# Kernel tuning notes

Hardware: AMD Instinct MI355X
Metric: run time of the kernel (lower is better)

Reference implementation:

```python
import jax, jax.numpy as jnp
import numpy as np
from jax import lax

B_SZ, SEQ, D_MODEL, D_STATE, DT_RANK = 4, 4096, 256, 16, 16


def setup_inputs() -> dict:
    key = jax.random.key(0)
    ks = jax.random.split(key, 12)
    d, n, r = D_MODEL, D_STATE, DT_RANK
    inp = {}
    inp["hidden_states"] = jax.random.normal(ks[0], (B_SZ, SEQ, d), jnp.float32)
    inp["in_proj_w"] = jax.random.normal(ks[1], (3 * d, d), jnp.float32) * (d ** -0.5)
    inp["x_proj_w"] = jax.random.normal(ks[2], (r + 2 * n, d), jnp.float32) * (d ** -0.5)
    s = r ** -0.5
    inp["dt_proj_w"] = jax.random.uniform(ks[3], (d, r), jnp.float32, -s, s)
    dt = jnp.exp(jax.random.uniform(ks[4], (d,), jnp.float32) * (np.log(0.1) - np.log(1e-3)) + np.log(1e-3))
    inp["dt_proj_b"] = dt + jnp.log(-jnp.expm1(-dt))  # inverse-softplus init
    inp["A_log"] = jnp.log(jnp.broadcast_to(jnp.arange(1, n + 1, dtype=jnp.float32), (d, n)))
    inp["D"] = jnp.ones((d,), jnp.float32)
    inp["out_proj1_w"] = jax.random.normal(ks[5], (d, d), jnp.float32) * (d ** -0.5)
    inp["conv_x_w"] = jax.random.normal(ks[6], (d, 1, 1), jnp.float32)
    inp["conv_x_b"] = jax.random.normal(ks[7], (d,), jnp.float32) * 0.1
    inp["conv_y_w"] = jax.random.normal(ks[8], (d, 1, 3), jnp.float32) * (3 ** -0.5)
    inp["conv_y_b"] = jax.random.normal(ks[9], (d,), jnp.float32) * 0.1
    inp["conv_z_w"] = jax.random.normal(ks[10], (d, 1, 5), jnp.float32) * (5 ** -0.5)
    inp["conv_z_b"] = jax.random.normal(ks[11], (d,), jnp.float32) * 0.1
    return inp


def _silu(x):
    return x * jax.nn.sigmoid(x)


def _dwconv(x, w, b):
    # x: (b, d, l); w: (d, 1, k) depthwise; 'same' padding (odd k)
    k = w.shape[-1]
    pad = (k - 1) // 2
    out = lax.conv_general_dilated(
        x, w, window_strides=(1,), padding=[(pad, pad)],
        dimension_numbers=("NCH", "OIH", "NCH"), feature_group_count=x.shape[1])
    return out + b[None, :, None]


def _selective_scan(u, delta, A, B, C, D, delta_bias):
    # u, delta: (b,d,l); A: (d,n); B,C: (b,n,l); D, delta_bias: (d,)
    delta = jax.nn.softplus(delta + delta_bias[None, :, None])
    dA = jnp.exp(jnp.einsum("bdl,dn->lbdn", delta, A))          # (l,b,d,n)
    dBu = jnp.einsum("bdl,bnl,bdl->lbdn", delta, B, u)           # (l,b,d,n)
    Ct = jnp.transpose(C, (2, 0, 1))                             # (l,b,n)

    def step(h, inp):
        dA_t, dBu_t, C_t = inp
        h = dA_t * h + dBu_t                                     # (b,d,n)
        y = jnp.einsum("bdn,bn->bd", h, C_t)
        return h, y

    h0 = jnp.zeros(u.shape[:2] + (A.shape[1],), u.dtype)
    _, ys = lax.scan(step, h0, (dA, dBu, Ct))                    # ys: (l,b,d)
    y = jnp.transpose(ys, (1, 2, 0))                             # (b,d,l)
    return y + D[None, :, None] * u


def reference(hidden_states, in_proj_w, x_proj_w, dt_proj_w, dt_proj_b, A_log, D,
              out_proj1_w, conv_x_w, conv_x_b, conv_y_w, conv_y_b, conv_z_w, conv_z_b):
    b, l, d = hidden_states.shape
    xyz = jnp.einsum("ble,de->bdl", hidden_states, in_proj_w)    # (b, 3d, l)
    x, y, z = jnp.split(xyz, 3, axis=1)                          # each (b,d,l)
    A = -jnp.exp(A_log.astype(jnp.float32))
    x = _silu(_dwconv(x, conv_x_w, conv_x_b))
    y = _silu(_dwconv(y, conv_y_w, conv_y_b))
    z = _silu(_dwconv(z, conv_z_w, conv_z_b))
    x_dbl = jnp.einsum("bdl,ed->ble", x, x_proj_w)               # (b,l,r+2n)
    dt_r, Bm, Cm = jnp.split(x_dbl, [DT_RANK, DT_RANK + D_STATE], axis=-1)
    # dt_proj applies bias here; selective_scan adds delta_bias again (faithful to source)
    dt = jnp.einsum("blr,dr->bdl", dt_r, dt_proj_w) + dt_proj_b[None, :, None]
    Bm = jnp.transpose(Bm, (0, 2, 1))                            # (b,n,l)
    Cm = jnp.transpose(Cm, (0, 2, 1))
    p = _selective_scan(x, dt, A, Bm, Cm, D.astype(jnp.float32), dt_proj_b.astype(jnp.float32))
    p = jnp.transpose(p, (0, 2, 1))                              # (b,l,d)
    y = jnp.transpose(y, (0, 2, 1))
    z = jnp.transpose(z, (0, 2, 1))
    l1 = jnp.einsum("bld,ed->ble", p * y, out_proj1_w)
    l2 = l1 * z
    l2 = _dwconv(jnp.transpose(l2, (0, 2, 1)), conv_x_w, conv_x_b)
    return jnp.transpose(l2, (0, 2, 1))                          # (b,l,d)
```

## Files before the change

### kernel.cpp

```cpp
#include <hip/hip_runtime.h>
#include <hip/hip_bf16.h>
#include <math.h>

typedef __hip_bfloat16 bf16;
typedef __attribute__((ext_vector_type(8))) short bf16x8;
typedef __attribute__((ext_vector_type(4))) float f32x4;

#define B_SZ 4
#define SEQ  4096
#define DM   256
#define NST  16
#define NCHK 64
#define LC   (SEQ/NCHK)
#define MT   (B_SZ*SEQ)
#define CT   4

__device__ __forceinline__ float silu_f(float v){ return v / (1.f + __expf(-v)); }
__device__ __forceinline__ float softplus_f(float v){
  return (v > 15.f) ? v : __logf(1.f + __expf(v));
}
__device__ __forceinline__ short f2bf(float f){
  union { bf16 h; short s; } u; u.h = __float2bfloat16(f); return u.s;
}
__device__ __forceinline__ float bf2f(short s){
  union { unsigned int i; float f; } v;
  v.i = ((unsigned int)(unsigned short)s) << 16; return v.f;
}
__device__ __forceinline__ float4 bf4_to_f4(uint2 q){
  float4 f;
  f.x = bf2f((short)(q.x & 0xffffu)); f.y = bf2f((short)(q.x >> 16));
  f.z = bf2f((short)(q.y & 0xffffu)); f.w = bf2f((short)(q.y >> 16));
  return f;
}
__device__ __forceinline__ short4 f4_to_bf4(float4 f){
  short4 s; s.x = f2bf(f.x); s.y = f2bf(f.y); s.z = f2bf(f.z); s.w = f2bf(f.w);
  return s;
}

template<int CTRL>
__device__ __forceinline__ float dpp_add_step(float v){
  int x = __builtin_amdgcn_update_dpp(0, __float_as_int(v), CTRL, 0xf, 0xf, true);
  return v + __int_as_float(x);
}

template<int EPI, bool A2M, bool ABF, bool OBF>
__global__ __launch_bounds__(256)
void mfma_gemm_k(const void* __restrict__ Av, const void* __restrict__ A2v,
                 const float* __restrict__ Bw, void* __restrict__ Outv,
                 int N, int K,
                 const float* __restrict__ bias, const short* __restrict__ zc,
                 const float* __restrict__ cwx)
{
  constexpr int BM = 128, BN = 128, BK = 32, LDP = 40;
  __shared__ short As[BM * LDP];
  __shared__ short Bs[BN * LDP];
  const int tid  = threadIdx.x;
  const int wave = tid >> 6, lane = tid & 63;
  const int quad = lane >> 4, l16 = lane & 15;
  const int wm = (wave & 1) * 64, wn = (wave >> 1) * 64;
  const int m0 = blockIdx.x * BM, n0 = blockIdx.y * BN;
  const int srow = tid >> 3;
  const int skq  = (tid & 7) * 4;

  f32x4 acc[4][4] = {};

  for (int k0 = 0; k0 < K; k0 += BK) {
    #pragma unroll
    for (int p = 0; p < 4; p++) {
      int row = p * 32 + srow;
      size_t ga = (size_t)(m0 + row) * K + k0 + skq;
      float4 q;
      if constexpr (ABF) q = bf4_to_f4(*(const uint2*)((const short*)Av + ga));
      else               q = *(const float4*)((const float*)Av + ga);
      if constexpr (A2M) {
        float4 r = bf4_to_f4(*(const uint2*)((const short*)A2v + ga));
        q.x *= r.x; q.y *= r.y; q.z *= r.z; q.w *= r.w;
      }
      *(short4*)&As[row * LDP + skq] = f4_to_bf4(q);
      size_t gb = (size_t)(n0 + row) * K + k0 + skq;
      *(short4*)&Bs[row * LDP + skq] = f4_to_bf4(*(const float4*)(Bw + gb));
    }
    __syncthreads();
    bf16x8 fa[4], fb[4];
    #pragma unroll
    for (int i = 0; i < 4; i++) {
      fa[i] = *(const bf16x8*)&As[(wm + i * 16 + l16) * LDP + quad * 8];
      fb[i] = *(const bf16x8*)&Bs[(wn + i * 16 + l16) * LDP + quad * 8];
    }
    #pragma unroll
    for (int i = 0; i < 4; i++)
      #pragma unroll
      for (int j = 0; j < 4; j++)
        acc[i][j] = __builtin_amdgcn_mfma_f32_16x16x32_bf16(fa[i], fb[j], acc[i][j], 0, 0, 0);
    __syncthreads();
  }

  #pragma unroll
  for (int i = 0; i < 4; i++) {
    #pragma unroll
    for (int j = 0; j < 4; j++) {
      int n = n0 + wn + j * 16 + l16;
      #pragma unroll
      for (int r = 0; r < 4; r++) {
        int m = m0 + wm + i * 16 + quad * 4 + r;
        float v = acc[i][j][r];
        if constexpr (EPI == 2)
          v = v * bf2f(zc[(size_t)m * N + n]) * cwx[n] + bias[n];
        if constexpr (OBF) ((short*)Outv)[(size_t)m * N + n] = f2bf(v);
        else               ((float*)Outv)[(size_t)m * N + n] = v;
      }
    }
  }
}

__global__ __launch_bounds__(256)
void gemm34_k(const short* __restrict__ xcb,
              const float* __restrict__ Bw,
              const float* __restrict__ wdt,
              const float* __restrict__ bdt,
              float* __restrict__ xdbl,
              float* __restrict__ dtv)
{
  constexpr int TM = 64, TK = 16, NN = 48;
  __shared__ __align__(16) float As[TK][TM + 4];
  __shared__ __align__(16) float Bs[TK][TM + 4];
  __shared__ __align__(16) float dt_s[TM][20];
  __shared__ __align__(16) float wdt_s[256][20];
  const int tid = threadIdx.x;
  const int tn = tid & 15, tm = tid >> 4;
  const int m0 = blockIdx.x * TM;
  float acc[4][4] = {};
  const int ml = tid >> 2;
  const int kq = (tid & 3) << 2;

  {
    float4 q0 = *(const float4*)&wdt[tid * 16 + 0];
    float4 q1 = *(const float4*)&wdt[tid * 16 + 4];
    float4 q2 = *(const float4*)&wdt[tid * 16 + 8];
    float4 q3 = *(const float4*)&wdt[tid * 16 + 12];
    *(float4*)&wdt_s[tid][0]  = q0;
    *(float4*)&wdt_s[tid][4]  = q1;
    *(float4*)&wdt_s[tid][8]  = q2;
    *(float4*)&wdt_s[tid][12] = q3;
  }

  for (int k0 = 0; k0 < 256; k0 += TK) {
    {
      size_t off = (size_t)(m0 + ml) * 256 + k0 + kq;
      float4 q = bf4_to_f4(*(const uint2*)(xcb + off));
      As[kq+0][ml] = q.x; As[kq+1][ml] = q.y; As[kq+2][ml] = q.z; As[kq+3][ml] = q.w;
    }
    {
      float v0 = 0.f, v1 = 0.f, v2 = 0.f, v3 = 0.f;
      if (ml < NN) {
        float4 q = *(const float4*)(Bw + (size_t)ml * 256 + k0 + kq);
        v0 = q.x; v1 = q.y; v2 = q.z; v3 = q.w;
      }
      Bs[kq+0][ml] = v0; Bs[kq+1][ml] = v1; Bs[kq+2][ml] = v2; Bs[kq+3][ml] = v3;
    }
    __syncthreads();
    #pragma unroll
    for (int k = 0; k < TK; k++) {
      float4 av = *(const float4*)&As[k][tm << 2];
      float4 bv = *(const float4*)&Bs[k][tn << 2];
      float a[4] = {av.x, av.y, av.z, av.w};
      float b[4] = {bv.x, bv.y, bv.z, bv.w};
      #pragma unroll
      for (int i = 0; i < 4; i++)
        #pragma unroll
        for (int j = 0; j < 4; j++)
          acc[i][j] = fmaf(a[i], b[j], acc[i][j]);
    }
    __syncthreads();
  }

  #pragma unroll
  for (int i = 0; i < 4; i++) {
    int m = m0 + (tm << 2) + i;
    #pragma unroll
    for (int j = 0; j < 4; j++) {
      int n = (tn << 2) + j;
      float v = acc[i][j];
      if (n < NN) xdbl[(size_t)m * NN + n] = v;
      if (tn < 4) dt_s[(tm << 2) + i][n] = v;
    }
  }
  __syncthreads();

  const int c0 = tid & 63, rg = tid >> 6;
  float w[4][16];
  float bb[4];
  #pragma unroll
  for (int cc = 0; cc < 4; cc++) {
    int col = cc * 64 + c0;
    #pragma unroll
    for (int q = 0; q < 4; q++) {
      float4 t = *(const float4*)&wdt_s[col][q * 4];
      w[cc][q*4+0] = t.x; w[cc][q*4+1] = t.y; w[cc][q*4+2] = t.z; w[cc][q*4+3] = t.w;
    }
    bb[cc] = 2.f * bdt[col];
  }
  #pragma unroll
  for (int rr = 0; rr < 16; rr++) {
    int row = rg * 16 + rr;
    float dr[16];
    #pragma unroll
    for (int q = 0; q < 4; q++) {
      float4 t = *(const float4*)&dt_s[row][q * 4];
      dr[q*4+0] = t.x; dr[q*4+1] = t.y; dr[q*4+2] = t.z; dr[q*4+3] = t.w;
    }
    #pragma unroll
    for (int cc = 0; cc < 4; cc++) {
      float s = bb[cc];
      #pragma unroll
      for (int k = 0; k < 16; k++) s = fmaf(dr[k], w[cc][k], s);
      dtv[(size_t)(m0 + row) * 256 + cc * 64 + c0] = softplus_f(s);
    }
  }
}

__global__ __launch_bounds__(256)
void conv_silu_k(const short* __restrict__ xyzb,
                 const float* __restrict__ wx, const float* __restrict__ bx,
                 const float* __restrict__ wy, const float* __restrict__ by,
                 const float* __restrict__ wz, const float* __restrict__ bz,
                 short* __restrict__ xcb, short* __restrict__ ycb,
                 short* __restrict__ zcb)
{
  int idx = blockIdx.x * 256 + threadIdx.x;
  int c4 = idx % 192;
  int lt = idx / 192;
  int row0 = lt * CT;
  int l0 = row0 & (SEQ - 1);

  float4 win[CT + 4];
  #pragma unroll
  for (int i = 0; i < CT + 4; i++) {
    int l = l0 + i - 2;
    if (l >= 0 && l < SEQ)
      win[i] = bf4_to_f4(*(const uint2*)(xyzb + (size_t)(row0 + i - 2) * 768 + c4 * 4));
    else
      win[i] = make_float4(0.f, 0.f, 0.f, 0.f);
  }

  if (c4 < 64) {
    int d = c4 * 4;
    float4 w  = *(const float4*)&wx[d];
    float4 bb = *(const float4*)&bx[d];
    #pragma unroll
    for (int t = 0; t < CT; t++) {
      float4 v = win[t + 2], o;
      o.x = silu_f(fmaf(v.x, w.x, bb.x));
      o.y = silu_f(fmaf(v.y, w.y, bb.y));
      o.z = silu_f(fmaf(v.z, w.z, bb.z));
      o.w = silu_f(fmaf(v.w, w.w, bb.w));
      *(short4*)&xcb[(size_t)(row0 + t) * 256 + d] = f4_to_bf4(o);
    }
  } else if (c4 < 128) {
    int d = (c4 - 64) * 4;
    float wq[4][3];
    #pragma unroll
    for (int q = 0; q < 4; q++)
      #pragma unroll
      for (int j = 0; j < 3; j++) wq[q][j] = wy[(d + q) * 3 + j];
    float4 bb = *(const float4*)&by[d];
    #pragma unroll
    for (int t = 0; t < CT; t++) {
      float a0 = bb.x, a1 = bb.y, a2 = bb.z, a3 = bb.w;
      #pragma unroll
      for (int j = 0; j < 3; j++) {
        float4 v = win[t + 1 + j];
        a0 = fmaf(v.x, wq[0][j], a0);
        a1 = fmaf(v.y, wq[1][j], a1);
        a2 = fmaf(v.z, wq[2][j], a2);
        a3 = fmaf(v.w, wq[3][j], a3);
      }
      float4 o; o.x = silu_f(a0); o.y = silu_f(a1); o.z = silu_f(a2); o.w = silu_f(a3);
      *(short4*)&ycb[(size_t)(row0 + t) * 256 + d] = f4_to_bf4(o);
    }
  } else {
    int d = (c4 - 128) * 4;
    float wq[4][5];
    #pragma unroll
    for (int q = 0; q < 4; q++)
      #pragma unroll
      for (int j = 0; j < 5; j++) wq[q][j] = wz[(d + q) * 5 + j];
    float4 bb = *(const float4*)&bz[d];
    #pragma unroll
    for (int t = 0; t < CT; t++) {
      float a0 = bb.x, a1 = bb.y, a2 = bb.z, a3 = bb.w;
      #pragma unroll
      for (int j = 0; j < 5; j++) {
        float4 v = win[t + j];
        a0 = fmaf(v.x, wq[0][j], a0);
        a1 = fmaf(v.y, wq[1][j], a1);
        a2 = fmaf(v.z, wq[2][j], a2);
        a3 = fmaf(v.w, wq[3][j], a3);
      }
      float4 o; o.x = silu_f(a0); o.y = silu_f(a1); o.z = silu_f(a2); o.w = silu_f(a3);
      *(short4*)&zcb[(size_t)(row0 + t) * 256 + d] = f4_to_bf4(o);
    }
  }
}

template<bool PASSC>
__global__ __launch_bounds__(256)
void scan_k(const short* __restrict__ xcb,
            const float* __restrict__ dtv,
            const float* __restrict__ xdbl,
            const float* __restrict__ A_log,
            const float* __restrict__ Dp,
            const float* __restrict__ Hstart,
            float* __restrict__ Pbuf, float* __restrict__ hfbuf,
            short* __restrict__ poutb)
{
  __shared__ __align__(16) float2 du2_s[16 * 66];
  __shared__ __align__(16) float2 BC_s [PASSC ? 16 * 66 : 2];
  __shared__ __align__(16) float  Bc_s [PASSC ? 4 : 16 * 68];
  __shared__ __align__(16) float  y_s  [PASSC ? 16 * 68 : 4];
  const int tid = threadIdx.x;
  const int n = tid & 15, dl = tid >> 4;
  const int ch = blockIdx.x;
  const int d0 = blockIdx.y * 16;
  const int b  = blockIdx.z;
  const int d  = d0 + dl;
  const int t0 = ch * LC;
  const size_t brow = (size_t)b * SEQ;

  float u_r[4];
  #pragma unroll
  for (int i = 0; i < 4; i++) {
    int t = (tid >> 4) + i * 16;
    int dd = tid & 15;
    size_t row = brow + t0 + t;
    float uval = bf2f(xcb[row * 256 + d0 + dd]);
    float dval = dtv[row * 256 + d0 + dd];
    du2_s[dd * 66 + t] = make_float2(dval, dval * uval);
    if constexpr (PASSC) {
      BC_s[dd * 66 + t] = make_float2(xdbl[row * 48 + 16 + dd],
                                      xdbl[row * 48 + 32 + dd]);
      u_r[i] = uval;
    } else {
      Bc_s[dd * 68 + t] = xdbl[row * 48 + 16 + dd];
    }
  }
  __syncthreads();

  const float A_dn = -__expf(A_log[d * NST + n]);
  const size_t cidx = (((size_t)b * DM + d) * NST + n) * NCHK + ch;

  float h = PASSC ? Hstart[cidx] : 0.f;
  float P = 1.f;
  for (int t4 = 0; t4 < LC; t4 += 4) {
    float4 a = *(const float4*)&du2_s[dl * 66 + t4];
    float4 c = *(const float4*)&du2_s[dl * 66 + t4 + 2];
    float dA[4], du[4];
    dA[0] = __expf(a.x * A_dn); du[0] = a.y;
    dA[1] = __expf(a.z * A_dn); du[1] = a.w;
    dA[2] = __expf(c.x * A_dn); du[2] = c.y;
    dA[3] = __expf(c.z * A_dn); du[3] = c.w;
    if constexpr (!PASSC) {
      float4 f = *(const float4*)&Bc_s[n * 68 + t4];
      float Bv[4] = {f.x, f.y, f.z, f.w};
      #pragma unroll
      for (int j = 0; j < 4; j++) {
        h = fmaf(dA[j], h, du[j] * Bv[j]);
        P *= dA[j];
      }
    } else {
      float4 e = *(const float4*)&BC_s[n * 66 + t4];
      float4 g = *(const float4*)&BC_s[n * 66 + t4 + 2];
      float Bv[4] = {e.x, e.z, g.x, g.z};
      float Cv[4] = {e.y, e.w, g.y, g.w};
      float yv[4];
      #pragma unroll
      for (int j = 0; j < 4; j++) {
        h = fmaf(dA[j], h, du[j] * Bv[j]);
        yv[j] = h * Cv[j];
      }
      #pragma unroll
      for (int j = 0; j < 4; j++) yv[j] = dpp_add_step<0x118>(yv[j]);
      #pragma unroll
      for (int j = 0; j < 4; j++) yv[j] = dpp_add_step<0x114>(yv[j]);
      #pragma unroll
      for (int j = 0; j < 4; j++) yv[j] = dpp_add_step<0x112>(yv[j]);
      #pragma unroll
      for (int j = 0; j < 4; j++) yv[j] = dpp_add_step<0x111>(yv[j]);
      if (n == 15)
        *(float4*)&y_s[dl * 68 + t4] = make_float4(yv[0], yv[1], yv[2], yv[3]);
    }
  }

  if constexpr (!PASSC) {
    Pbuf[cidx] = P;
    hfbuf[cidx] = h;
  } else {
    __syncthreads();
    const float Dval = Dp[d0 + n];
    #pragma unroll
    for (int i = 0; i < 4; i++) {
      int t = (tid >> 4) + i * 16;
      poutb[(brow + t0 + t) * 256 + d0 + n] =
          f2bf(fmaf(Dval, u_r[i], y_s[n * 68 + t]));
    }
  }
}

__global__ __launch_bounds__(256)
void scan_mid_k(const float* __restrict__ Pbuf, const float* __restrict__ hfbuf,
                float* __restrict__ Hstart)
{
  int tid = blockIdx.x * 256 + threadIdx.x;
  size_t base = (size_t)tid * NCHK;
  float H = 0.f;
  for (int c = 0; c < NCHK; c++) {
    Hstart[base + c] = H;
    H = Pbuf[base + c] * H + hfbuf[base + c];
  }
}

extern "C" void kernel_launch(void* const* d_in, const int* in_sizes, int n_in,
                              void* d_out, int out_size, void* d_ws, size_t ws_size,
                              hipStream_t stream)
{
  const float* hs    = (const float*)d_in[0];
  const float* w_in  = (const float*)d_in[1];
  const float* w_xp  = (const float*)d_in[2];
  const float* w_dt  = (const float*)d_in[3];
  const float* b_dt  = (const float*)d_in[4];
  const float* A_log = (const float*)d_in[5];
  const float* Dp    = (const float*)d_in[6];
  const float* w_o1  = (const float*)d_in[7];
  const float* cwx   = (const float*)d_in[8];
  const float* cbx   = (const float*)d_in[9];
  const float* cwy   = (const float*)d_in[10];
  const float* cby   = (const float*)d_in[11];
  const float* cwz   = (const float*)d_in[12];
  const float* cbz   = (const float*)d_in[13];

  char* wsb = (char*)d_ws;
  short* xyzb = (short*)wsb;
  short* xcb  = (short*)(wsb + (size_t)MT * 768 * 2);
  short* ycb  = xcb + (size_t)MT * 256;
  short* zcb  = ycb + (size_t)MT * 256;
  short* pbufb= zcb + (size_t)MT * 256;
  float* xdbl = (float*)(pbufb + (size_t)MT * 256);
  float* dtv  = xdbl + (size_t)MT * 48;
  float* Pb   = dtv  + (size_t)MT * 256;
  float* hf   = Pb   + (size_t)B_SZ * DM * NST * NCHK;
  float* Hs   = hf   + (size_t)B_SZ * DM * NST * NCHK;

  dim3 blk(256);

  mfma_gemm_k<0, false, false, true><<<dim3(MT / 128, 768 / 128), blk, 0, stream>>>(
      hs, nullptr, w_in, xyzb, 768, 256, nullptr, nullptr, nullptr);

  conv_silu_k<<<dim3((MT / CT) * 192 / 256), blk, 0, stream>>>(
      xyzb, cwx, cbx, cwy, cby, cwz, cbz, xcb, ycb, zcb);

  gemm34_k<<<dim3(MT / 64), blk, 0, stream>>>(
      xcb, w_xp, w_dt, b_dt, xdbl, dtv);

  scan_k<false><<<dim3(NCHK, DM / 16, B_SZ), blk, 0, stream>>>(
      xcb, dtv, xdbl, A_log, Dp, nullptr, Pb, hf, nullptr);
  scan_mid_k<<<dim3((B_SZ * DM * NST) / 256), blk, 0, stream>>>(Pb, hf, Hs);
  scan_k<true><<<dim3(NCHK, DM / 16, B_SZ), blk, 0, stream>>>(
      xcb, dtv, xdbl, A_log, Dp, Hs, nullptr, nullptr, pbufb);

  mfma_gemm_k<2, true, true, false><<<dim3(MT / 128, 256 / 128), blk, 0, stream>>>(
      pbufb, ycb, w_o1, (float*)d_out, 256, 256, cbx, zcb, cwx);
}
```

Baseline: 219.3 us.

## Pre-convert GEMM weights to bf16, fuse y-gate into scan, shrink gemm34 tiles

A new small kernel converts the in-proj and out-proj weights to bf16 once per call. The MFMA GEMM then loads both operands with 16-byte copies and no per-tile conversion. The y gating multiply moves into the scan's output stage, so the final GEMM reads only one bf16 activation instead of two. gemm34 now uses 32-row tiles, doubling the grid for better occupancy, at the cost of reloading the weights more often and one extra kernel launch.

Result: faster. 208.6 us (-4.9%).

```diff
diff --git a/kernel.cpp b/kernel.cpp
--- a/kernel.cpp
+++ b/kernel.cpp
@@ -43,11 +43,25 @@
   return v + __int_as_float(x);
 }
 
-template<int EPI, bool A2M, bool ABF, bool OBF>
 __global__ __launch_bounds__(256)
-void mfma_gemm_k(const void* __restrict__ Av, const void* __restrict__ A2v,
-                 const float* __restrict__ Bw, void* __restrict__ Outv,
-                 int N, int K,
+void cvt_w_k(const float* __restrict__ w_in, const float* __restrict__ w_o1,
+             short* __restrict__ w_in_b, short* __restrict__ w_o1_b)
+{
+  int i = blockIdx.x * 256 + threadIdx.x;
+  if (i < 49152) {
+    float4 q = *(const float4*)&w_in[i * 4];
+    *(short4*)&w_in_b[i * 4] = f4_to_bf4(q);
+  } else {
+    int j = i - 49152;
+    float4 q = *(const float4*)&w_o1[j * 4];
+    *(short4*)&w_o1_b[j * 4] = f4_to_bf4(q);
+  }
+}
+
+template<int EPI, bool ABF, bool OBF>
+__global__ __launch_bounds__(256)
+void mfma_gemm_k(const void* __restrict__ Av, const short* __restrict__ Bw,
+                 void* __restrict__ Outv, int N, int K,
                  const float* __restrict__ bias, const short* __restrict__ zc,
                  const float* __restrict__ cwx)
 {
@@ -61,24 +75,35 @@
   const int m0 = blockIdx.x * BM, n0 = blockIdx.y * BN;
   const int srow = tid >> 3;
   const int skq  = (tid & 7) * 4;
+  const int crow = tid >> 2;
+  const int cck  = (tid & 3) * 8;
 
   f32x4 acc[4][4] = {};
 
   for (int k0 = 0; k0 < K; k0 += BK) {
-    #pragma unroll
-    for (int p = 0; p < 4; p++) {
-      int row = p * 32 + srow;
-      size_t ga = (size_t)(m0 + row) * K + k0 + skq;
-      float4 q;
-      if constexpr (ABF) q = bf4_to_f4(*(const uint2*)((const short*)Av + ga));
-      else               q = *(const float4*)((const float*)Av + ga);
-      if constexpr (A2M) {
-        float4 r = bf4_to_f4(*(const uint2*)((const short*)A2v + ga));
-        q.x *= r.x; q.y *= r.y; q.z *= r.z; q.w *= r.w;
-      }
-      *(short4*)&As[row * LDP + skq] = f4_to_bf4(q);
-      size_t gb = (size_t)(n0 + row) * K + k0 + skq;
-      *(short4*)&Bs[row * LDP + skq] = f4_to_bf4(*(const float4*)(Bw + gb));
+    if constexpr (ABF) {
+      #pragma unroll
+      for (int p = 0; p < 2; p++) {
+        int row = p * 64 + crow;
+        uint4 v = *(const uint4*)((const short*)Av + (size_t)(m0 + row) * K + k0 + cck);
+        *(uint4*)&As[row * LDP + cck] = v;
+      }
+    } else {
+      #pragma unroll
+      for (int p = 0; p < 4; p++) {
+        int row = p * 32 + srow;
+        size_t ga = (size_t)(m0 + row) * K + k0 + skq;
+        float4 q = *(const float4*)((const float*)Av + ga);
+        *(short4*)&As[row * LDP + skq] = f4_to_bf4(q);
+      }
+    }
+    {
+      #pragma unroll
+      for (int p = 0; p < 2; p++) {
+        int row = p * 64 + crow;
+        uint4 v = *(const uint4*)(Bw + (size_t)(n0 + row) * K + k0 + cck);
+        *(uint4*)&Bs[row * LDP + cck] = v;
+      }
     }
     __syncthreads();
     bf16x8 fa[4], fb[4];
@@ -121,17 +146,17 @@
               float* __restrict__ xdbl,
               float* __restrict__ dtv)
 {
-  constexpr int TM = 64, TK = 16, NN = 48;
+  constexpr int TM = 32, TK = 16, NN = 48;
   __shared__ __align__(16) float As[TK][TM + 4];
-  __shared__ __align__(16) float Bs[TK][TM + 4];
+  __shared__ __align__(16) float Bs[TK][64 + 4];
   __shared__ __align__(16) float dt_s[TM][20];
   __shared__ __align__(16) float wdt_s[256][20];
   const int tid = threadIdx.x;
   const int tn = tid & 15, tm = tid >> 4;
   const int m0 = blockIdx.x * TM;
-  float acc[4][4] = {};
-  const int ml = tid >> 2;
-  const int kq = (tid & 3) << 2;
+  float acc[2][4] = {};
+  const int mlA = tid >> 3, kdA = (tid & 7) * 2;
+  const int mlB = tid >> 2, kqB = (tid & 3) * 4;
 
   {
     float4 q0 = *(const float4*)&wdt[tid * 16 + 0];
@@ -146,27 +171,28 @@
 
   for (int k0 = 0; k0 < 256; k0 += TK) {
     {
-      size_t off = (size_t)(m0 + ml) * 256 + k0 + kq;
-      float4 q = bf4_to_f4(*(const uint2*)(xcb + off));
-      As[kq+0][ml] = q.x; As[kq+1][ml] = q.y; As[kq+2][ml] = q.z; As[kq+3][ml] = q.w;
+      size_t off = (size_t)(m0 + mlA) * 256 + k0 + kdA;
+      unsigned int v = *(const unsigned int*)(xcb + off);
+      As[kdA + 0][mlA] = bf2f((short)(v & 0xffffu));
+      As[kdA + 1][mlA] = bf2f((short)(v >> 16));
     }
     {
       float v0 = 0.f, v1 = 0.f, v2 = 0.f, v3 = 0.f;
-      if (ml < NN) {
-        float4 q = *(const float4*)(Bw + (size_t)ml * 256 + k0 + kq);
+      if (mlB < NN) {
+        float4 q = *(const float4*)(Bw + (size_t)mlB * 256 + k0 + kqB);
         v0 = q.x; v1 = q.y; v2 = q.z; v3 = q.w;
       }
-      Bs[kq+0][ml] = v0; Bs[kq+1][ml] = v1; Bs[kq+2][ml] = v2; Bs[kq+3][ml] = v3;
+      Bs[kqB+0][mlB] = v0; Bs[kqB+1][mlB] = v1; Bs[kqB+2][mlB] = v2; Bs[kqB+3][mlB] = v3;
     }
     __syncthreads();
     #pragma unroll
     for (int k = 0; k < TK; k++) {
-      float4 av = *(const float4*)&As[k][tm << 2];
+      float2 av = *(const float2*)&As[k][tm << 1];
       float4 bv = *(const float4*)&Bs[k][tn << 2];
-      float a[4] = {av.x, av.y, av.z, av.w};
+      float a[2] = {av.x, av.y};
       float b[4] = {bv.x, bv.y, bv.z, bv.w};
       #pragma unroll
-      for (int i = 0; i < 4; i++)
+      for (int i = 0; i < 2; i++)
         #pragma unroll
         for (int j = 0; j < 4; j++)
           acc[i][j] = fmaf(a[i], b[j], acc[i][j]);
@@ -175,14 +201,14 @@
   }
 
   #pragma unroll
-  for (int i = 0; i < 4; i++) {
-    int m = m0 + (tm << 2) + i;
+  for (int i = 0; i < 2; i++) {
+    int m = m0 + (tm << 1) + i;
     #pragma unroll
     for (int j = 0; j < 4; j++) {
       int n = (tn << 2) + j;
       float v = acc[i][j];
       if (n < NN) xdbl[(size_t)m * NN + n] = v;
-      if (tn < 4) dt_s[(tm << 2) + i][n] = v;
+      if (tn < 4) dt_s[(tm << 1) + i][n] = v;
     }
   }
   __syncthreads();
@@ -201,8 +227,8 @@
     bb[cc] = 2.f * bdt[col];
   }
   #pragma unroll
-  for (int rr = 0; rr < 16; rr++) {
-    int row = rg * 16 + rr;
+  for (int rr = 0; rr < 8; rr++) {
+    int row = rg * 8 + rr;
     float dr[16];
     #pragma unroll
     for (int q = 0; q < 4; q++) {
@@ -312,6 +338,7 @@
             const float* __restrict__ Dp,
             const float* __restrict__ Hstart,
             float* __restrict__ Pbuf, float* __restrict__ hfbuf,
+            const short* __restrict__ ycb,
             short* __restrict__ poutb)
 {
   __shared__ __align__(16) float2 du2_s[16 * 66];
@@ -400,8 +427,10 @@
     #pragma unroll
     for (int i = 0; i < 4; i++) {
       int t = (tid >> 4) + i * 16;
-      poutb[(brow + t0 + t) * 256 + d0 + n] =
-          f2bf(fmaf(Dval, u_r[i], y_s[n * 68 + t]));
+      size_t row = brow + t0 + t;
+      float p = fmaf(Dval, u_r[i], y_s[n * 68 + t]);
+      float yg = bf2f(ycb[row * 256 + d0 + n]);
+      poutb[row * 256 + d0 + n] = f2bf(p * yg);
     }
   }
 }
@@ -444,7 +473,9 @@
   short* ycb  = xcb + (size_t)MT * 256;
   short* zcb  = ycb + (size_t)MT * 256;
   short* pbufb= zcb + (size_t)MT * 256;
-  float* xdbl = (float*)(pbufb + (size_t)MT * 256);
+  short* w_in_b = pbufb + (size_t)MT * 256;
+  short* w_o1_b = w_in_b + 768 * 256;
+  float* xdbl = (float*)(w_o1_b + 256 * 256 + 128);
   float* dtv  = xdbl + (size_t)MT * 48;
   float* Pb   = dtv  + (size_t)MT * 256;
   float* hf   = Pb   + (size_t)B_SZ * DM * NST * NCHK;
@@ -452,21 +483,23 @@
 
   dim3 blk(256);
 
-  mfma_gemm_k<0, false, false, true><<<dim3(MT / 128, 768 / 128), blk, 0, stream>>>(
-      hs, nullptr, w_in, xyzb, 768, 256, nullptr, nullptr, nullptr);
+  cvt_w_k<<<dim3(256), blk, 0, stream>>>(w_in, w_o1, w_in_b, w_o1_b);
+
+  mfma_gemm_k<0, false, true><<<dim3(MT / 128, 768 / 128), blk, 0, stream>>>(
+      hs, w_in_b, xyzb, 768, 256, nullptr, nullptr, nullptr);
 
   conv_silu_k<<<dim3((MT / CT) * 192 / 256), blk, 0, stream>>>(
       xyzb, cwx, cbx, cwy, cby, cwz, cbz, xcb, ycb, zcb);
 
-  gemm34_k<<<dim3(MT / 64), blk, 0, stream>>>(
+  gemm34_k<<<dim3(MT / 32), blk, 0, stream>>>(
       xcb, w_xp, w_dt, b_dt, xdbl, dtv);
 
   scan_k<false><<<dim3(NCHK, DM / 16, B_SZ), blk, 0, stream>>>(
-      xcb, dtv, xdbl, A_log, Dp, nullptr, Pb, hf, nullptr);
+      xcb, dtv, xdbl, A_log, Dp, nullptr, Pb, hf, nullptr, nullptr);
   scan_mid_k<<<dim3((B_SZ * DM * NST) / 256), blk, 0, stream>>>(Pb, hf, Hs);
   scan_k<true><<<dim3(NCHK, DM / 16, B_SZ), blk, 0, stream>>>(
-      xcb, dtv, xdbl, A_log, Dp, Hs, nullptr, nullptr, pbufb);
-
-  mfma_gemm_k<2, true, true, false><<<dim3(MT / 128, 256 / 128), blk, 0, stream>>>(
-      pbufb, ycb, w_o1, (float*)d_out, 256, 256, cbx, zcb, cwx);
-}
+      xcb, dtv, xdbl, A_log, Dp, Hs, nullptr, nullptr, ycb, pbufb);
+
+  mfma_gemm_k<2, true, false><<<dim3(MT / 128, 256 / 128), blk, 0, stream>>>(
+      pbufb, w_o1_b, d_out, 256, 256, cbx, zcb, cwx);
+}
```
